# Kernel optimization log

Hardware: AMD Instinct MI355X
Metric: run time of the kernel (lower is better)

The kernel has to match this reference:

```python
import jax, jax.numpy as jnp
import numpy as np

MIN_RES = np.array([16, 16, 16, 16], dtype=np.float64)
MAX_RES = np.array([256, 256, 256, 128], dtype=np.float64)
NUM_SCALES = 16
MAX_PARAMS = 2 ** 19
FEATS = 2
B = 131072
PRIMES = np.array([1, 2654435761, 805459861, 3674653429], dtype=np.uint64)


def _level_meta():
    # replicates HashEncoderHyFluid.__init__ table layout
    b = np.exp((np.log(MAX_RES) - np.log(MIN_RES)) / (NUM_SCALES - 1))
    shapes, sizes, ind, offs = [], [], [], []
    total = 0
    for s in range(NUM_SCALES):
        res = np.ceil(MIN_RES * np.power(b, s)).astype(int)
        raw = np.int64(res[0] + 1) * np.int64(res[1] + 1) * np.int64(res[2] + 1) * np.int64(res[3] + 1)
        p = int(raw) if raw % 8 == 0 else int((raw + 8 - 1) / 8) * 8
        p = min(MAX_PARAMS, p)
        shapes.append(res)
        sizes.append(p)
        ind.append(1 if raw <= p else 0)
        offs.append(total)
        total += p * FEATS
    return (np.array(shapes, np.int32), np.array(sizes, np.uint32),
            np.array(ind, np.int32), np.array(offs, np.int32), total)


def setup_inputs() -> dict:
    key = jax.random.key(0)
    k1, k2 = jax.random.split(key)
    shapes, sizes, ind, offs, total = _level_meta()
    xyzts = jax.random.uniform(k1, (B, 4), dtype=jnp.float32)
    table = (jax.random.uniform(k2, (total,), dtype=jnp.float32) * 2.0 - 1.0) * 1e-4
    return {
        'xyzts': xyzts,
        'table': table,
        'shapes': jnp.asarray(shapes, jnp.int32),
        'sizes': jnp.asarray(sizes, jnp.uint32),
        'indicator': jnp.asarray(ind, jnp.int32),
        'offsets': jnp.asarray(offs, jnp.int32),
    }


def _encode(xyzts, table, shapes, sizes, indicator, offsets):
    n, L = xyzts.shape[0], shapes.shape[0]
    resf = shapes.astype(jnp.float32)                      # [L,4]
    pos = xyzts[:, None, :] * resf[None]                   # [B,L,4]
    grid_f = jnp.clip(jnp.floor(pos), 0.0, resf[None] - 1.0)
    frac = jnp.clip(pos - grid_f, 0.0, 1.0)                # [B,L,4]
    grid = grid_f.astype(jnp.uint32)                       # [B,L,4]
    # under_hash strides: prod_{i<d}(res[i]+1), uint32 wrap like taichi
    res1 = (shapes + 1).astype(jnp.uint32)                 # [L,4]
    strides = jnp.concatenate(
        [jnp.ones((L, 1), jnp.uint32), jnp.cumprod(res1[:, :3], axis=1)], axis=1)  # [L,4]
    bits = ((jnp.arange(16)[:, None] >> jnp.arange(4)[None, :]) & 1)  # [16,4]
    bits_u = bits.astype(jnp.uint32)
    w = jnp.ones((1, 1, 16), dtype=pos.dtype)
    fast = jnp.zeros((n, L, 16), jnp.uint32)
    under = jnp.zeros((n, L, 16), jnp.uint32)
    for d in range(4):  # static unroll over the 4 coordinate dims
        c = grid[:, :, None, d] + bits_u[None, None, :, d]          # [B,L,16]
        t = frac[:, :, None, d]                                     # [B,L,1]
        w = w * jnp.where(bits[None, None, :, d] == 1, t, 1.0 - t)  # [B,L,16]
        fast = fast ^ (c * jnp.uint32(int(PRIMES[d])))
        under = under + c * strides[None, :, None, d]
    h = jnp.where(indicator[None, :, None] == 1, under, fast) % sizes[None, :, None]
    it = offsets[None, :, None] + h.astype(jnp.int32) * 2           # [B,L,16]
    f0 = table[it]
    f1 = table[it + 1]
    out0 = jnp.sum(w * f0, axis=-1)                                 # [B,L]
    out1 = jnp.sum(w * f1, axis=-1)                                 # [B,L]
    return jnp.stack([out0, out1], axis=-1).reshape(n, L * 2)


def reference(xyzts, table, shapes, sizes, indicator, offsets):
    return _encode(xyzts, table, shapes, sizes, indicator, offsets)
```

## Files before the change

### kernel.cpp

```cpp
#include <hip/hip_runtime.h>

#define PRIME1 2654435761u
#define PRIME2 805459861u
#define PRIME3 3674653429u

typedef float f2v __attribute__((ext_vector_type(2)));
typedef float f4v __attribute__((ext_vector_type(4)));

template <bool DIRECT>
__global__ __launch_bounds__(256) void hash_enc_kernel(
    const float* __restrict__ xyzts,
    const float* __restrict__ table,
    const int* __restrict__ shapes,
    const unsigned int* __restrict__ sizes,
    const int* __restrict__ indicator,
    const int* __restrict__ offsets,
    float* __restrict__ dst,
    int npts, int nchunks)
{
    int b = blockIdx.x;
    int half = b / (nchunks * 8);
    int within = b % (nchunks * 8);
    int level = (within & 7) + (half << 3);
    int chunk = within >> 3;
    int n = chunk * 256 + (int)threadIdx.x;
    if (n >= npts) return;

    int4 rs = reinterpret_cast<const int4*>(shapes)[level];
    unsigned int size = sizes[level];
    unsigned int msk = size - 1u;
    bool ind = (indicator[level] != 0);
    int off = offsets[level];

    f4v x = __builtin_nontemporal_load(
        reinterpret_cast<const f4v*>(xyzts) + n);

    float r0 = (float)rs.x, r1 = (float)rs.y, r2 = (float)rs.z, r3 = (float)rs.w;
    float p0 = x.x * r0, p1 = x.y * r1, p2 = x.z * r2, p3 = x.w * r3;
    float g0 = fminf(fmaxf(floorf(p0), 0.f), r0 - 1.f);
    float g1 = fminf(fmaxf(floorf(p1), 0.f), r1 - 1.f);
    float g2 = fminf(fmaxf(floorf(p2), 0.f), r2 - 1.f);
    float g3 = fminf(fmaxf(floorf(p3), 0.f), r3 - 1.f);
    float f0 = fminf(fmaxf(p0 - g0, 0.f), 1.f);
    float f1 = fminf(fmaxf(p1 - g1, 0.f), 1.f);
    float f2 = fminf(fmaxf(p2 - g2, 0.f), 1.f);
    float f3 = fminf(fmaxf(p3 - g3, 0.f), 1.f);
    unsigned int u0 = (unsigned int)g0, u1 = (unsigned int)g1;
    unsigned int u2 = (unsigned int)g2, u3 = (unsigned int)g3;

    unsigned int s1 = (unsigned int)(rs.x + 1);
    unsigned int s2 = s1 * (unsigned int)(rs.y + 1);
    unsigned int s3 = s2 * (unsigned int)(rs.z + 1);

    unsigned int a1 = u1 * PRIME1, a2 = u2 * PRIME2, a3 = u3 * PRIME3;
    unsigned int xb = u0 ^ a1 ^ a2 ^ a3;
    unsigned int e0 = u0 ^ (u0 + 1u);
    unsigned int e1 = a1 ^ ((u1 + 1u) * PRIME1);
    unsigned int e2 = a2 ^ ((u2 + 1u) * PRIME2);
    unsigned int e3 = a3 ^ ((u3 + 1u) * PRIME3);

    unsigned int ab = u0 + u1 * s1 + u2 * s2 + u3 * s3;

    float om0 = 1.f - f0, om1 = 1.f - f1, om2 = 1.f - f2, om3 = 1.f - f3;

    const float* tb = table + off;

    unsigned int idx[16];
#pragma unroll
    for (int c = 0; c < 16; ++c) {
        unsigned int hf = xb, hu = ab;
        if (c & 1) { hf ^= e0; hu += 1u; }
        if (c & 2) { hf ^= e1; hu += s1; }
        if (c & 4) { hf ^= e2; hu += s2; }
        if (c & 8) { hf ^= e3; hu += s3; }
        idx[c] = ind ? hu : (hf & msk);
    }

    f2v v[16];
#pragma unroll
    for (int c = 0; c < 16; ++c)
        v[c] = *reinterpret_cast<const f2v*>(tb + 2u * idx[c]);

    float acc0 = 0.f, acc1 = 0.f;
#pragma unroll
    for (int c = 0; c < 16; ++c) {
        float w = (c & 1) ? f0 : om0;
        w *= (c & 2) ? f1 : om1;
        w *= (c & 4) ? f2 : om2;
        w *= (c & 8) ? f3 : om3;
        acc0 += w * v[c].x;
        acc1 += w * v[c].y;
    }

    f2v res;
    res.x = acc0; res.y = acc1;
    if (DIRECT) {
        reinterpret_cast<f2v*>(dst)[(size_t)n * 16 + level] = res;
    } else {
        __builtin_nontemporal_store(
            res, reinterpret_cast<f2v*>(dst) + (size_t)level * npts + n);
    }
}

__global__ __launch_bounds__(256) void transpose_kernel(
    const float* __restrict__ ws, float* __restrict__ out, int npts)
{
    int n = blockIdx.x * 256 + (int)threadIdx.x;
    if (n >= npts) return;
    const f2v* w = reinterpret_cast<const f2v*>(ws);
    f2v v[16];
#pragma unroll
    for (int l = 0; l < 16; ++l)
        v[l] = w[(size_t)l * npts + n];
    f4v* o = reinterpret_cast<f4v*>(out + (size_t)n * 32);
#pragma unroll
    for (int j = 0; j < 8; ++j) {
        f4v q;
        q.x = v[2 * j].x; q.y = v[2 * j].y;
        q.z = v[2 * j + 1].x; q.w = v[2 * j + 1].y;
        __builtin_nontemporal_store(q, o + j);
    }
}

extern "C" void kernel_launch(void* const* d_in, const int* in_sizes, int n_in,
                              void* d_out, int out_size, void* d_ws, size_t ws_size,
                              hipStream_t stream) {
    const float* xyzts = (const float*)d_in[0];
    const float* table = (const float*)d_in[1];
    const int* shapes = (const int*)d_in[2];
    const unsigned int* sizes = (const unsigned int*)d_in[3];
    const int* indicator = (const int*)d_in[4];
    const int* offsets = (const int*)d_in[5];
    float* out = (float*)d_out;

    int npts = in_sizes[0] / 4;
    int nchunks = (npts + 255) / 256;
    int blocks = nchunks * 16;

    size_t ws_needed = (size_t)npts * 16 * 2 * sizeof(float);
    if (ws_size >= ws_needed) {
        float* ws = (float*)d_ws;
        hash_enc_kernel<false><<<blocks, 256, 0, stream>>>(
            xyzts, table, shapes, sizes, indicator, offsets, ws, npts, nchunks);
        transpose_kernel<<<nchunks, 256, 0, stream>>>(ws, out, npts);
    } else {
        hash_enc_kernel<true><<<blocks, 256, 0, stream>>>(
            xyzts, table, shapes, sizes, indicator, offsets, out, npts, nchunks);
    }
}
```

Measured before the change: 131.2 us.

## Rebalance heavy-level tail blocks across XCDs and widen transpose to two points per thread

For the exact test shape (512 chunks of 256 points), the main grid stops doing the last 64 chunks of levels 11-15. Extra appended blocks pick that work up, and the block index is chosen so those blocks land only on XCD slots 0-2. The aim is to even out per-XCD load caused by the costly large hash levels. The transpose is also replaced by a version that reads float4 (two points per level) and writes two output rows per thread, cutting the number of load instructions. The rebalancing only applies to the hardcoded size, assumes round-robin block placement on XCDs, and launches many blocks that exit immediately.

```diff
diff --git a/kernel.cpp b/kernel.cpp
--- a/kernel.cpp
+++ b/kernel.cpp
@@ -16,13 +16,26 @@
     const int* __restrict__ indicator,
     const int* __restrict__ offsets,
     float* __restrict__ dst,
-    int npts, int nchunks)
+    int npts, int nchunks, int rebalance)
 {
     int b = blockIdx.x;
-    int half = b / (nchunks * 8);
-    int within = b % (nchunks * 8);
-    int level = (within & 7) + (half << 3);
-    int chunk = within >> 3;
+    int main_blocks = nchunks * 16;
+    int level, chunk;
+    if (b >= main_blocks) {
+        int i = b - main_blocks;
+        int r = i & 7;
+        if (r >= 3) return;
+        int w = (i >> 3) * 3 + r;
+        if (w >= 320) return;
+        level = 11 + (w >> 6);
+        chunk = 448 + (w & 63);
+    } else {
+        int half = b / (nchunks * 8);
+        int within = b % (nchunks * 8);
+        level = (within & 7) + (half << 3);
+        chunk = within >> 3;
+        if (rebalance && level >= 11 && chunk >= 448) return;
+    }
     int n = chunk * 256 + (int)threadIdx.x;
     if (n >= npts) return;
 
@@ -102,6 +115,31 @@
     }
 }
 
+__global__ __launch_bounds__(256) void transpose2_kernel(
+    const float* __restrict__ ws, float* __restrict__ out, int npts)
+{
+    int t = blockIdx.x * 256 + (int)threadIdx.x;
+    int n0 = t * 2;
+    if (n0 >= npts) return;
+    int hp = npts >> 1;
+    const f4v* w = reinterpret_cast<const f4v*>(ws);
+    f4v v[16];
+#pragma unroll
+    for (int l = 0; l < 16; ++l)
+        v[l] = __builtin_nontemporal_load(w + (size_t)l * hp + t);
+    f4v* o = reinterpret_cast<f4v*>(out + (size_t)n0 * 32);
+#pragma unroll
+    for (int j = 0; j < 8; ++j) {
+        f4v q0, q1;
+        q0.x = v[2 * j].x; q0.y = v[2 * j].y;
+        q0.z = v[2 * j + 1].x; q0.w = v[2 * j + 1].y;
+        q1.x = v[2 * j].z; q1.y = v[2 * j].w;
+        q1.z = v[2 * j + 1].z; q1.w = v[2 * j + 1].w;
+        __builtin_nontemporal_store(q0, o + j);
+        __builtin_nontemporal_store(q1, o + 8 + j);
+    }
+}
+
 __global__ __launch_bounds__(256) void transpose_kernel(
     const float* __restrict__ ws, float* __restrict__ out, int npts)
 {
@@ -135,16 +173,24 @@
 
     int npts = in_sizes[0] / 4;
     int nchunks = (npts + 255) / 256;
-    int blocks = nchunks * 16;
+    int rebalance = (nchunks == 512 && npts == nchunks * 256) ? 1 : 0;
+    int blocks = nchunks * 16 + (rebalance ? 107 * 8 : 0);
 
     size_t ws_needed = (size_t)npts * 16 * 2 * sizeof(float);
     if (ws_size >= ws_needed) {
         float* ws = (float*)d_ws;
         hash_enc_kernel<false><<<blocks, 256, 0, stream>>>(
-            xyzts, table, shapes, sizes, indicator, offsets, ws, npts, nchunks);
-        transpose_kernel<<<nchunks, 256, 0, stream>>>(ws, out, npts);
+            xyzts, table, shapes, sizes, indicator, offsets, ws, npts, nchunks,
+            rebalance);
+        if ((npts & 1) == 0) {
+            int t = npts >> 1;
+            transpose2_kernel<<<(t + 255) / 256, 256, 0, stream>>>(ws, out, npts);
+        } else {
+            transpose_kernel<<<nchunks, 256, 0, stream>>>(ws, out, npts);
+        }
     } else {
         hash_enc_kernel<true><<<blocks, 256, 0, stream>>>(
-            xyzts, table, shapes, sizes, indicator, offsets, out, npts, nchunks);
+            xyzts, table, shapes, sizes, indicator, offsets, out, npts, nchunks,
+            rebalance);
     }
 }
```

Result: slower. 146.1 us (+11.3%).
